# Optimization experiments

Hardware: AMD Instinct MI355X
Metric: run time of the kernel (lower is better)

## Reference

```python
import jax, jax.numpy as jnp
import numpy as np

N_NODES = 50000
HEADS1 = 4
NEG_SLOPE = 0.2
EPS = 1e-16


def gat_conv(x, edge_index, W, att_src, att_dst, bias, heads, out_ch, concat):
    # edge_index: [2, E] with self-loops already appended by caller
    src, dst = edge_index[0], edge_index[1]
    N = x.shape[0]
    h = (x @ W).reshape(N, heads, out_ch)                      # [N, H, C]
    a_src = jnp.sum(h * att_src, axis=-1)                      # [N, H]
    a_dst = jnp.sum(h * att_dst, axis=-1)                      # [N, H]
    e = a_src[src] + a_dst[dst]                                # [E, H]
    e = jnp.where(e > 0, e, NEG_SLOPE * e)                     # leaky_relu
    m = jax.ops.segment_max(e, dst, num_segments=N)            # [N, H]
    alpha = jnp.exp(e - m[dst])                                # [E, H]
    denom = jax.ops.segment_sum(alpha, dst, num_segments=N)    # [N, H]
    alpha = alpha / (denom[dst] + EPS)                         # [E, H]
    msg = alpha[:, :, None] * h[src]                           # [E, H, C]
    out = jax.ops.segment_sum(msg, dst, num_segments=N)        # [N, H, C]
    if concat:
        out = out.reshape(N, heads * out_ch)
    else:
        out = out.mean(axis=1)
    return out + bias, alpha


def setup_inputs() -> dict:
    key = jax.random.key(0)
    ks = jax.random.split(key, 12)
    N, F, H, heads, C, E = N_NODES, 256, 64, HEADS1, 40, 800000
    g = 0.1
    return {
        "x": jax.random.normal(ks[0], (N, F), dtype=jnp.float32),
        "edge_index": jax.random.randint(ks[1], (2, E), 0, N, dtype=jnp.int32),
        "W1": jax.random.normal(ks[2], (F, heads * H), dtype=jnp.float32) * g,
        "att_src1": jax.random.normal(ks[3], (heads, H), dtype=jnp.float32) * g,
        "att_dst1": jax.random.normal(ks[4], (heads, H), dtype=jnp.float32) * g,
        "b1": jnp.zeros((heads * H,), dtype=jnp.float32),
        "W2": jax.random.normal(ks[5], (heads * H, C), dtype=jnp.float32) * g,
        "att_src2": jax.random.normal(ks[6], (1, C), dtype=jnp.float32) * g,
        "att_dst2": jax.random.normal(ks[7], (1, C), dtype=jnp.float32) * g,
        "b2": jnp.zeros((C,), dtype=jnp.float32),
    }


def reference(x, edge_index, W1, att_src1, att_dst1, b1, W2, att_src2, att_dst2, b2):
    N = x.shape[0]
    # add self-loops (PyG GATConv default)
    loops = jnp.arange(N, dtype=edge_index.dtype)
    ei = jnp.concatenate([edge_index, jnp.stack([loops, loops])], axis=1)
    # dropout is identity in eval mode
    h1, alpha = gat_conv(x, ei, W1, att_src1, att_dst1, b1,
                         HEADS1, W1.shape[1] // HEADS1, concat=True)
    h1 = jax.nn.elu(h1)
    h2, _ = gat_conv(h1, ei, W2, att_src2, att_dst2, b2,
                     1, W2.shape[1], concat=False)
    return jax.nn.log_softmax(h2, axis=1), alpha
```

## Files before the change

### kernel.cpp

```cpp
#include <hip/hip_runtime.h>
#include <math.h>

#define N_NODES 50000
#define HC1 256
#define H1 4
#define C2 40
#define C2P 64
#define E0 800000
#define ET 850000
#define NEG_SLOPE 0.2f
#define EPS_A 1e-16f

typedef __bf16 bf16x8 __attribute__((ext_vector_type(8)));
typedef float f32x4 __attribute__((ext_vector_type(4)));
typedef unsigned short u16x8 __attribute__((ext_vector_type(8)));


__device__ inline unsigned short f2bf(float f) {
    unsigned u = __float_as_uint(f);
    return (unsigned short)((u + 0x7FFFu + ((u >> 16) & 1u)) >> 16);
}
__device__ inline float bf_lo(unsigned q) { return __uint_as_float(q << 16); }
__device__ inline float bf_hi(unsigned q) { return __uint_as_float(q & 0xFFFF0000u); }


__global__ void fill_int_kernel(int* __restrict__ p, int n, int v) {
    int i = blockIdx.x * blockDim.x + threadIdx.x;
    if (i < n) p[i] = v;
}

__device__ inline int edge_src(const int* __restrict__ ei, int e) {
    return (e < E0) ? ei[e] : (e - E0);
}
__device__ inline int edge_dst(const int* __restrict__ ei, int e) {
    return (e < E0) ? ei[E0 + e] : (e - E0);
}


#define CV_X 3200000
#define CV_W1 65536
#define CV_W2 16384

__global__ void convert_all_kernel(const float* __restrict__ x,
                                   const float* __restrict__ W1,
                                   const float* __restrict__ W2,
                                   ushort4* __restrict__ xbf,
                                   unsigned short* __restrict__ w1t,
                                   unsigned short* __restrict__ w2t) {
    int tid = blockIdx.x * blockDim.x + threadIdx.x;
    if (tid < CV_X) {
        float4 v = ((const float4*)x)[tid];
        ushort4 w;
        w.x = f2bf(v.x); w.y = f2bf(v.y); w.z = f2bf(v.z); w.w = f2bf(v.w);
        xbf[tid] = w;
    } else if (tid < CV_X + CV_W1) {
        int i = tid - CV_X;
        int n = i >> 8, k = i & 255;
        w1t[i] = f2bf(W1[k * 256 + n]);
    } else if (tid < CV_X + CV_W1 + CV_W2) {
        int i = tid - CV_X - CV_W1;
        int n = i >> 8, k = i & 255;
        w2t[i] = (n < C2) ? f2bf(W2[k * C2 + n]) : (unsigned short)0;
    }
}


__global__ void hist_kernel(const int* __restrict__ ei, int* __restrict__ deg) {
    int e = blockIdx.x * blockDim.x + threadIdx.x;
    if (e >= ET) return;
    atomicAdd(&deg[edge_dst(ei, e)], 1);
}

__global__ __launch_bounds__(256) void scan_block_kernel(const int* __restrict__ deg,
                                                         int* __restrict__ excl,
                                                         int* __restrict__ bsum) {
    __shared__ int tmp[256];
    int t = threadIdx.x;
    int i = blockIdx.x * 256 + t;
    int v = (i < N_NODES) ? deg[i] : 0;
    tmp[t] = v;
    __syncthreads();
#pragma unroll
    for (int o = 1; o < 256; o <<= 1) {
        int x = (t >= o) ? tmp[t - o] : 0;
        __syncthreads();
        tmp[t] += x;
        __syncthreads();
    }
    if (i < N_NODES) excl[i] = tmp[t] - v;
    if (t == 255) bsum[blockIdx.x] = tmp[255];
}

#define NSCAN_B 196

__global__ __launch_bounds__(256) void scan_top_kernel(int* __restrict__ bsum) {
    __shared__ int tmp[256];
    int t = threadIdx.x;
    int v = (t < NSCAN_B) ? bsum[t] : 0;
    tmp[t] = v;
    __syncthreads();
#pragma unroll
    for (int o = 1; o < 256; o <<= 1) {
        int x = (t >= o) ? tmp[t - o] : 0;
        __syncthreads();
        tmp[t] += x;
        __syncthreads();
    }
    if (t < NSCAN_B) bsum[t] = tmp[t] - v;
}

__global__ __launch_bounds__(256) void scan_add_kernel(int* __restrict__ offsets,
                                                       int* __restrict__ cursor,
                                                       const int* __restrict__ bsum) {
    int i = blockIdx.x * 256 + threadIdx.x;
    if (i < N_NODES) {
        int v = offsets[i] + bsum[blockIdx.x];
        offsets[i] = v;
        cursor[i] = v;
    }
    if (i == 0) offsets[N_NODES] = ET;
}

__global__ void scatter_kernel(const int* __restrict__ ei, int* __restrict__ cursor,
                               int2* __restrict__ csr_es) {
    int e = blockIdx.x * blockDim.x + threadIdx.x;
    if (e >= ET) return;
    int d = edge_dst(ei, e);
    int pos = atomicAdd(&cursor[d], 1);
    csr_es[pos] = make_int2(e, edge_src(ei, e));
}


template <int TBM, int TBN, int WROWS, int WCOLS>
__global__ __launch_bounds__(256) void gemm_mfma_kernel(const unsigned short* __restrict__ Abf,
                                                        const unsigned short* __restrict__ Bt,
                                                        unsigned short* __restrict__ Cbf,
                                                        const float* __restrict__ att_s,
                                                        const float* __restrict__ att_d,
                                                        float* __restrict__ a_src_o,
                                                        float* __restrict__ a_dst_o,
                                                        int M, int Nc, int attN, int hstride) {
    static_assert(TBM == WROWS * 64 && TBN == WCOLS * 64, "tile");
    constexpr int LDK = 40;
    __shared__ alignas(16) unsigned short As[TBM * LDK];
    __shared__ alignas(16) unsigned short Bs[TBN * LDK];
    const int t = threadIdx.x;
    const int lane = t & 63;
    const int w = t >> 6;
    const int quad = lane >> 4;
    const int l16 = lane & 15;
    const int wm = (w / WCOLS) * 64;
    const int wn = (w % WCOLS) * 64;
    const int bm = blockIdx.x * TBM;
    const int bn = blockIdx.y * TBN;

    f32x4 acc[4][4] = {};

    for (int k0 = 0; k0 < 256; k0 += 32) {
        __syncthreads();
#pragma unroll
        for (int i = 0; i < TBM / 64; ++i) {
            int idx = t + i * 256;
            int row = idx >> 2, seg = idx & 3;
            u16x8 v = {};
            if (bm + row < M)
                v = *(const u16x8*)(Abf + (size_t)(bm + row) * 256 + k0 + seg * 8);
            *(u16x8*)&As[row * LDK + seg * 8] = v;
        }
#pragma unroll
        for (int i = 0; i < TBN / 64; ++i) {
            int idx = t + i * 256;
            int row = idx >> 2, seg = idx & 3;
            u16x8 v = *(const u16x8*)(Bt + (size_t)(bn + row) * 256 + k0 + seg * 8);
            *(u16x8*)&Bs[row * LDK + seg * 8] = v;
        }
        __syncthreads();

        bf16x8 af[4], bfr[4];
#pragma unroll
        for (int mi = 0; mi < 4; ++mi)
            af[mi] = *(const bf16x8*)&As[(wm + mi * 16 + l16) * LDK + quad * 8];
#pragma unroll
        for (int ni = 0; ni < 4; ++ni)
            bfr[ni] = *(const bf16x8*)&Bs[(wn + ni * 16 + l16) * LDK + quad * 8];
#pragma unroll
        for (int mi = 0; mi < 4; ++mi)
#pragma unroll
            for (int ni = 0; ni < 4; ++ni)
                acc[mi][ni] = __builtin_amdgcn_mfma_f32_16x16x32_bf16(
                    af[mi], bfr[ni], acc[mi][ni], 0, 0, 0);
    }

#pragma unroll
    for (int mi = 0; mi < 4; ++mi)
#pragma unroll
        for (int ni = 0; ni < 4; ++ni)
#pragma unroll
            for (int r = 0; r < 4; ++r) {
                int row = bm + wm + mi * 16 + quad * 4 + r;
                int col = bn + wn + ni * 16 + l16;
                if (row < M)
                    Cbf[(size_t)row * Nc + col] = f2bf(acc[mi][ni][r]);
            }

    float asc[4], adc[4];
#pragma unroll
    for (int ni = 0; ni < 4; ++ni) {
        int col = bn + wn + ni * 16 + l16;
        bool valid = col < attN;
        asc[ni] = valid ? att_s[col] : 0.f;
        adc[ni] = valid ? att_d[col] : 0.f;
    }
    float vs[16], vd[16];
#pragma unroll
    for (int mi = 0; mi < 4; ++mi)
#pragma unroll
        for (int r = 0; r < 4; ++r) {
            float s = 0.f, dd = 0.f;
#pragma unroll
            for (int ni = 0; ni < 4; ++ni) {
                s += acc[mi][ni][r] * asc[ni];
                dd += acc[mi][ni][r] * adc[ni];
            }
            vs[mi * 4 + r] = s;
            vd[mi * 4 + r] = dd;
        }
#pragma unroll
    for (int k = 0; k < 4; ++k) {
        const int o = 1 << k;
        const int b = (l16 >> k) & 1;
#pragma unroll
        for (int j = 0; j < (8 >> k); ++j) {
            float lo = vs[2 * j], hi = vs[2 * j + 1];
            float keep = b ? hi : lo, send = b ? lo : hi;
            vs[j] = keep + __shfl_xor(send, o);
            lo = vd[2 * j]; hi = vd[2 * j + 1];
            keep = b ? hi : lo; send = b ? lo : hi;
            vd[j] = keep + __shfl_xor(send, o);
        }
    }
    {
        int mi = l16 >> 2, r = l16 & 3;
        int row = bm + wm + mi * 16 + quad * 4 + r;
        int head = (bn + wn) >> 6;
        if (row < M) {
            a_src_o[(size_t)row * hstride + head] = vs[0];
            a_dst_o[(size_t)row * hstride + head] = vd[0];
        }
    }
}


__global__ __launch_bounds__(256) void l1_fused_kernel(const int* __restrict__ off,
                                                       const int2* __restrict__ csr_es,
                                                       const float4* __restrict__ a_src4,
                                                       const float4* __restrict__ a_dst4,
                                                       const unsigned* __restrict__ h1bf,
                                                       const float* __restrict__ b1,
                                                       float4* __restrict__ alpha_out4,
                                                       unsigned* __restrict__ out1bf) {
    __shared__ int    s_w[4][64];
    __shared__ float4 a_w[4][64];
    int t = threadIdx.x;
    int w = t >> 6, lane = t & 63;
    int d = blockIdx.x * 4 + w;
    int beg = off[d], end = off[d + 1];
    int deg = end - beg;
    int nch = (deg + 63) >> 6;
    int cnt0 = min(deg, 64);
    bool act0 = lane < cnt0;
    float4 ad4 = a_dst4[d];

    int2  es0 = make_int2(0, 0);
    float4 l0 = make_float4(-INFINITY, -INFINITY, -INFINITY, -INFINITY);
    float4 mx = l0;
    for (int cc = 0; cc < nch; ++cc) {
        int idx = beg + cc * 64 + lane;
        float4 l = make_float4(-INFINITY, -INFINITY, -INFINITY, -INFINITY);
        int2 es = make_int2(0, 0);
        if (idx < end) {
            es = csr_es[idx];
            float4 as4 = a_src4[es.y];
            l.x = as4.x + ad4.x; l.x = l.x > 0.f ? l.x : NEG_SLOPE * l.x;
            l.y = as4.y + ad4.y; l.y = l.y > 0.f ? l.y : NEG_SLOPE * l.y;
            l.z = as4.z + ad4.z; l.z = l.z > 0.f ? l.z : NEG_SLOPE * l.z;
            l.w = as4.w + ad4.w; l.w = l.w > 0.f ? l.w : NEG_SLOPE * l.w;
        }
        if (cc == 0) { es0 = es; l0 = l; }
        mx.x = fmaxf(mx.x, l.x); mx.y = fmaxf(mx.y, l.y);
        mx.z = fmaxf(mx.z, l.z); mx.w = fmaxf(mx.w, l.w);
    }
    int rdeg = cnt0;
    for (int o = 1; o < rdeg; o <<= 1) {
        mx.x = fmaxf(mx.x, __shfl_xor(mx.x, o));
        mx.y = fmaxf(mx.y, __shfl_xor(mx.y, o));
        mx.z = fmaxf(mx.z, __shfl_xor(mx.z, o));
        mx.w = fmaxf(mx.w, __shfl_xor(mx.w, o));
    }
    mx.x = __shfl(mx.x, 0); mx.y = __shfl(mx.y, 0);
    mx.z = __shfl(mx.z, 0); mx.w = __shfl(mx.w, 0);

    float4 p0 = make_float4(0.f, 0.f, 0.f, 0.f);
    if (act0) {
        p0.x = __expf(l0.x - mx.x); p0.y = __expf(l0.y - mx.y);
        p0.z = __expf(l0.z - mx.z); p0.w = __expf(l0.w - mx.w);
    }
    float4 sum = p0;
    for (int cc = 1; cc < nch; ++cc) {
        int idx = beg + cc * 64 + lane;
        if (idx < end) {
            int2 es = csr_es[idx];
            float4 as4 = a_src4[es.y];
            float4 l;
            l.x = as4.x + ad4.x; l.x = l.x > 0.f ? l.x : NEG_SLOPE * l.x;
            l.y = as4.y + ad4.y; l.y = l.y > 0.f ? l.y : NEG_SLOPE * l.y;
            l.z = as4.z + ad4.z; l.z = l.z > 0.f ? l.z : NEG_SLOPE * l.z;
            l.w = as4.w + ad4.w; l.w = l.w > 0.f ? l.w : NEG_SLOPE * l.w;
            sum.x += __expf(l.x - mx.x); sum.y += __expf(l.y - mx.y);
            sum.z += __expf(l.z - mx.z); sum.w += __expf(l.w - mx.w);
        }
    }
    for (int o = 1; o < rdeg; o <<= 1) {
        sum.x += __shfl_xor(sum.x, o);
        sum.y += __shfl_xor(sum.y, o);
        sum.z += __shfl_xor(sum.z, o);
        sum.w += __shfl_xor(sum.w, o);
    }
    sum.x = __shfl(sum.x, 0); sum.y = __shfl(sum.y, 0);
    sum.z = __shfl(sum.z, 0); sum.w = __shfl(sum.w, 0);
    float4 inv;
    inv.x = 1.f / (sum.x + EPS_A); inv.y = 1.f / (sum.y + EPS_A);
    inv.z = 1.f / (sum.z + EPS_A); inv.w = 1.f / (sum.w + EPS_A);

    float4 al0;
    al0.x = p0.x * inv.x; al0.y = p0.y * inv.y;
    al0.z = p0.z * inv.z; al0.w = p0.w * inv.w;
    if (act0) {
        alpha_out4[es0.x] = al0;
        s_w[w][lane] = es0.y;
        a_w[w][lane] = al0;
    }
    __syncthreads();

    int head = lane >> 4;
    int base2 = 2 * lane;
    const float* aw = (const float*)&a_w[w][0];
    float4 acc = make_float4(0.f, 0.f, 0.f, 0.f);
    int j = 0;
    for (; j + 4 <= cnt0; j += 4) {
        int s0 = s_w[w][j], s1 = s_w[w][j + 1], s2 = s_w[w][j + 2], s3 = s_w[w][j + 3];
        float A0 = aw[4 * j + head], A1 = aw[4 * j + 4 + head];
        float A2 = aw[4 * j + 8 + head], A3 = aw[4 * j + 12 + head];
        uint2 q0 = *(const uint2*)&h1bf[(size_t)s0 * 128 + base2];
        uint2 q1 = *(const uint2*)&h1bf[(size_t)s1 * 128 + base2];
        uint2 q2 = *(const uint2*)&h1bf[(size_t)s2 * 128 + base2];
        uint2 q3 = *(const uint2*)&h1bf[(size_t)s3 * 128 + base2];
        acc.x += A0 * bf_lo(q0.x) + A1 * bf_lo(q1.x) + A2 * bf_lo(q2.x) + A3 * bf_lo(q3.x);
        acc.y += A0 * bf_hi(q0.x) + A1 * bf_hi(q1.x) + A2 * bf_hi(q2.x) + A3 * bf_hi(q3.x);
        acc.z += A0 * bf_lo(q0.y) + A1 * bf_lo(q1.y) + A2 * bf_lo(q2.y) + A3 * bf_lo(q3.y);
        acc.w += A0 * bf_hi(q0.y) + A1 * bf_hi(q1.y) + A2 * bf_hi(q2.y) + A3 * bf_hi(q3.y);
    }
    for (; j < cnt0; ++j) {
        int s = s_w[w][j];
        float A = aw[4 * j + head];
        uint2 q = *(const uint2*)&h1bf[(size_t)s * 128 + base2];
        acc.x += A * bf_lo(q.x); acc.y += A * bf_hi(q.x);
        acc.z += A * bf_lo(q.y); acc.w += A * bf_hi(q.y);
    }

    for (int cc = 1; cc < nch; ++cc) {
        int idx = beg + cc * 64 + lane;
        int ms = 0;
        float4 ma = make_float4(0.f, 0.f, 0.f, 0.f);
        if (idx < end) {
            int2 es = csr_es[idx];
            ms = es.y;
            float4 as4 = a_src4[es.y];
            float4 l;
            l.x = as4.x + ad4.x; l.x = l.x > 0.f ? l.x : NEG_SLOPE * l.x;
            l.y = as4.y + ad4.y; l.y = l.y > 0.f ? l.y : NEG_SLOPE * l.y;
            l.z = as4.z + ad4.z; l.z = l.z > 0.f ? l.z : NEG_SLOPE * l.z;
            l.w = as4.w + ad4.w; l.w = l.w > 0.f ? l.w : NEG_SLOPE * l.w;
            ma.x = __expf(l.x - mx.x) * inv.x;
            ma.y = __expf(l.y - mx.y) * inv.y;
            ma.z = __expf(l.z - mx.z) * inv.z;
            ma.w = __expf(l.w - mx.w) * inv.w;
            alpha_out4[es.x] = ma;
        }
        int cnt = min(64, deg - cc * 64);
        for (int jj = 0; jj < cnt; ++jj) {
            int s = __shfl(ms, jj);
            float h0 = __shfl(ma.x, jj), h1 = __shfl(ma.y, jj);
            float h2 = __shfl(ma.z, jj), h3 = __shfl(ma.w, jj);
            float A = (head & 2) ? ((head & 1) ? h3 : h2) : ((head & 1) ? h1 : h0);
            uint2 q = *(const uint2*)&h1bf[(size_t)s * 128 + base2];
            acc.x += A * bf_lo(q.x); acc.y += A * bf_hi(q.x);
            acc.z += A * bf_lo(q.y); acc.w += A * bf_hi(q.y);
        }
    }

    float4 bb = *(const float4*)&b1[4 * lane];
    float v0 = acc.x + bb.x, v1 = acc.y + bb.y, v2 = acc.z + bb.z, v3 = acc.w + bb.w;
    v0 = v0 > 0.f ? v0 : __expf(v0) - 1.f;
    v1 = v1 > 0.f ? v1 : __expf(v1) - 1.f;
    v2 = v2 > 0.f ? v2 : __expf(v2) - 1.f;
    v3 = v3 > 0.f ? v3 : __expf(v3) - 1.f;
    uint2 qo;
    qo.x = ((unsigned)f2bf(v1) << 16) | (unsigned)f2bf(v0);
    qo.y = ((unsigned)f2bf(v3) << 16) | (unsigned)f2bf(v2);
    *(uint2*)&out1bf[(size_t)d * 128 + base2] = qo;
}


__global__ __launch_bounds__(256) void l2_fused_kernel(const int* __restrict__ off,
                                                       const int2* __restrict__ csr_es,
                                                       const float* __restrict__ a_src,
                                                       const float* __restrict__ a_dst,
                                                       const unsigned* __restrict__ h2bf,
                                                       const float* __restrict__ b2,
                                                       float* __restrict__ out) {
    int t = threadIdx.x;
    int lane = t & 63;
    int d = blockIdx.x * 4 + (t >> 6);
    if (d >= N_NODES) return;
    int beg = off[d], end = off[d + 1];
    int deg = end - beg;
    float ad = a_dst[d];
    int nch = (deg + 63) >> 6;

    float elc[4]; int sc[4];
    float mx = -INFINITY;
    for (int cc = 0; cc < nch; ++cc) {
        int idx = beg + cc * 64 + lane;
        float el = -INFINITY; int s = 0;
        if (idx < end) {
            int2 es = csr_es[idx];
            s = es.y;
            el = a_src[s] + ad;
            el = el > 0.f ? el : NEG_SLOPE * el;
        }
        if (cc < 4) { elc[cc] = el; sc[cc] = s; }
        mx = fmaxf(mx, el);
    }
    int rdeg = min(deg, 64);
    for (int o = 1; o < rdeg; o <<= 1) mx = fmaxf(mx, __shfl_xor(mx, o));
    mx = __shfl(mx, 0);

    float sum = 0.f;
    for (int cc = 0; cc < nch; ++cc) {
        int idx = beg + cc * 64 + lane;
        float p = 0.f;
        if (cc < 4) {
            p = (idx < end) ? __expf(elc[cc] - mx) : 0.f;
            elc[cc] = p;
        } else if (idx < end) {
            int2 es = csr_es[idx];
            float el = a_src[es.y] + ad;
            el = el > 0.f ? el : NEG_SLOPE * el;
            p = __expf(el - mx);
        }
        sum += p;
    }
    for (int o = 1; o < rdeg; o <<= 1) sum += __shfl_xor(sum, o);
    sum = __shfl(sum, 0);
    float inv = 1.f / (sum + EPS_A);

    int half = lane >> 5, li = lane & 31;
    float acc0 = 0.f, acc1 = 0.f;
    for (int cc = 0; cc < nch; ++cc) {
        int cnt = min(64, deg - cc * 64);
        int my_s; float my_a;
        if (cc < 4) {
            my_s = sc[cc];
            my_a = elc[cc];
        } else {
            int idx = beg + cc * 64 + lane;
            my_s = 0; my_a = 0.f;
            if (idx < end) {
                int2 es = csr_es[idx];
                my_s = es.y;
                float el = a_src[es.y] + ad;
                el = el > 0.f ? el : NEG_SLOPE * el;
                my_a = __expf(el - mx);
            }
        }
        for (int j = 0; j < cnt; j += 2) {
            int jj = j + half;
            int s = __shfl(my_s, jj);
            float a = __shfl(my_a, jj);
            if (jj < cnt) {
                unsigned q = h2bf[(size_t)s * 32 + li];
                acc0 += a * bf_lo(q);
                acc1 += a * bf_hi(q);
            }
        }
    }
    acc0 += __shfl_xor(acc0, 32);
    acc1 += __shfl_xor(acc1, 32);
    acc0 *= inv;
    acc1 *= inv;
    bool act = li < 20;
    float v0 = act ? acc0 + b2[2 * li]     : -INFINITY;
    float v1 = act ? acc1 + b2[2 * li + 1] : -INFINITY;
    float mmx = fmaxf(v0, v1);
#pragma unroll
    for (int o = 16; o; o >>= 1) mmx = fmaxf(mmx, __shfl_xor(mmx, o));
    float ex = act ? __expf(v0 - mmx) + __expf(v1 - mmx) : 0.f;
#pragma unroll
    for (int o = 16; o; o >>= 1) ex += __shfl_xor(ex, o);
    float ls = __logf(ex);
    if (act && half == 0)
        *(float2*)&out[(size_t)d * C2 + 2 * li] = make_float2(v0 - mmx - ls, v1 - mmx - ls);
}


extern "C" void kernel_launch(void* const* d_in, const int* in_sizes, int n_in,
                              void* d_out, int out_size, void* d_ws, size_t ws_size,
                              hipStream_t stream) {
    const float* x   = (const float*)d_in[0];
    const int*   ei  = (const int*)d_in[1];
    const float* W1  = (const float*)d_in[2];
    const float* as1 = (const float*)d_in[3];
    const float* ad1 = (const float*)d_in[4];
    const float* b1  = (const float*)d_in[5];
    const float* W2  = (const float*)d_in[6];
    const float* as2 = (const float*)d_in[7];
    const float* ad2 = (const float*)d_in[8];
    const float* b2  = (const float*)d_in[9];

    float* out   = (float*)d_out;
    float* alpha = out + (size_t)N_NODES * C2;

    unsigned* u32    = (unsigned*)d_ws;
    unsigned* h1bf   = u32;
    unsigned* xbf    = h1bf + 6400000;
    unsigned* h2bf   = xbf + 6400000;
    unsigned* w1t    = h2bf + 1600000;
    unsigned* w2t    = w1t + 32768;
    float* a_src1    = (float*)(w2t + 8192);
    float* a_dst1    = a_src1 + 200000;
    float* a_src2    = a_dst1 + 200000;
    float* a_dst2    = a_src2 + 50000;
    int*   deg       = (int*)(a_dst2 + 50000);
    int*   offs      = deg + 50000;
    int*   cursor    = offs + 50001;
    int*   bsum      = cursor + 50000;
    int2*  csr_es    = (int2*)(bsum + 257);
    unsigned* out1bf = xbf;

    const int TB = 256;
    const int EB = (ET + TB - 1) / TB;

    fill_int_kernel<<<(N_NODES + TB - 1) / TB, TB, 0, stream>>>(deg, N_NODES, 0);
    hist_kernel<<<EB, TB, 0, stream>>>(ei, deg);
    scan_block_kernel<<<NSCAN_B, TB, 0, stream>>>(deg, offs, bsum);
    scan_top_kernel<<<1, TB, 0, stream>>>(bsum);
    scan_add_kernel<<<NSCAN_B, TB, 0, stream>>>(offs, cursor, bsum);
    scatter_kernel<<<EB, TB, 0, stream>>>(ei, cursor, csr_es);

    convert_all_kernel<<<(CV_X + CV_W1 + CV_W2 + TB - 1) / TB, TB, 0, stream>>>(
        x, W1, W2, (ushort4*)xbf, (unsigned short*)w1t, (unsigned short*)w2t);

    gemm_mfma_kernel<128, 128, 2, 2><<<dim3((N_NODES + 127) / 128, 2), TB, 0, stream>>>(
        (const unsigned short*)xbf, (const unsigned short*)w1t, (unsigned short*)h1bf,
        as1, ad1, a_src1, a_dst1, N_NODES, HC1, 256, H1);
    l1_fused_kernel<<<N_NODES / 4, TB, 0, stream>>>(offs, csr_es,
                                                    (const float4*)a_src1,
                                                    (const float4*)a_dst1,
                                                    h1bf, b1, (float4*)alpha, out1bf);

    gemm_mfma_kernel<256, 64, 4, 1><<<dim3((N_NODES + 255) / 256, 1), TB, 0, stream>>>(
        (const unsigned short*)out1bf, (const unsigned short*)w2t, (unsigned short*)h2bf,
        as2, ad2, a_src2, a_dst2, N_NODES, C2P, C2, 1);
    l2_fused_kernel<<<(N_NODES + 3) / 4, TB, 0, stream>>>(offs, csr_es, a_src2, a_dst2,
                                                          h2bf, b2, out);
}
```

Baseline: 382.0 us.

## Split GAT aggregation across half-waves with wider loads and fuse degree zeroing

In layer-1 aggregation each half-wave now handles alternate edges and loads 16-byte rows (8 bf16 per lane), with a cross-half shuffle reduction at the end. The layer-2 kernel merges the softmax-sum and aggregation passes into one pass, staging (src, p) pairs in LDS so neighbor rows can be fetched two at a time. The degree-zeroing fill kernel is folded into the conversion kernel to remove one launch. These changes aim to raise memory-level parallelism and cut redundant passes over the edges, at the cost of an extra reduction, some LDS traffic, and a layer-2 kernel that no longer guards d >= N_NODES (safe only because N_NODES is divisible by 4).

```diff
diff --git a/kernel.cpp b/kernel.cpp
--- a/kernel.cpp
+++ b/kernel.cpp
@@ -24,11 +24,6 @@
 __device__ inline float bf_hi(unsigned q) { return __uint_as_float(q & 0xFFFF0000u); }
 
 
-__global__ void fill_int_kernel(int* __restrict__ p, int n, int v) {
-    int i = blockIdx.x * blockDim.x + threadIdx.x;
-    if (i < n) p[i] = v;
-}
-
 __device__ inline int edge_src(const int* __restrict__ ei, int e) {
     return (e < E0) ? ei[e] : (e - E0);
 }
@@ -40,13 +35,15 @@
 #define CV_X 3200000
 #define CV_W1 65536
 #define CV_W2 16384
+#define CV_TOT (CV_X + CV_W1 + CV_W2 + N_NODES)
 
 __global__ void convert_all_kernel(const float* __restrict__ x,
                                    const float* __restrict__ W1,
                                    const float* __restrict__ W2,
                                    ushort4* __restrict__ xbf,
                                    unsigned short* __restrict__ w1t,
-                                   unsigned short* __restrict__ w2t) {
+                                   unsigned short* __restrict__ w2t,
+                                   int* __restrict__ deg) {
     int tid = blockIdx.x * blockDim.x + threadIdx.x;
     if (tid < CV_X) {
         float4 v = ((const float4*)x)[tid];
@@ -61,6 +58,8 @@
         int i = tid - CV_X - CV_W1;
         int n = i >> 8, k = i & 255;
         w2t[i] = (n < C2) ? f2bf(W2[k * C2 + n]) : (unsigned short)0;
+    } else if (tid < CV_TOT) {
+        deg[tid - CV_X - CV_W1 - CV_W2] = 0;
     }
 }
 
@@ -342,30 +341,33 @@
     }
     __syncthreads();
 
-    int head = lane >> 4;
-    int base2 = 2 * lane;
+    int hf = lane >> 5, li = lane & 31;
+    int headc = li >> 3;
     const float* aw = (const float*)&a_w[w][0];
-    float4 acc = make_float4(0.f, 0.f, 0.f, 0.f);
-    int j = 0;
-    for (; j + 4 <= cnt0; j += 4) {
-        int s0 = s_w[w][j], s1 = s_w[w][j + 1], s2 = s_w[w][j + 2], s3 = s_w[w][j + 3];
-        float A0 = aw[4 * j + head], A1 = aw[4 * j + 4 + head];
-        float A2 = aw[4 * j + 8 + head], A3 = aw[4 * j + 12 + head];
-        uint2 q0 = *(const uint2*)&h1bf[(size_t)s0 * 128 + base2];
-        uint2 q1 = *(const uint2*)&h1bf[(size_t)s1 * 128 + base2];
-        uint2 q2 = *(const uint2*)&h1bf[(size_t)s2 * 128 + base2];
-        uint2 q3 = *(const uint2*)&h1bf[(size_t)s3 * 128 + base2];
-        acc.x += A0 * bf_lo(q0.x) + A1 * bf_lo(q1.x) + A2 * bf_lo(q2.x) + A3 * bf_lo(q3.x);
-        acc.y += A0 * bf_hi(q0.x) + A1 * bf_hi(q1.x) + A2 * bf_hi(q2.x) + A3 * bf_hi(q3.x);
-        acc.z += A0 * bf_lo(q0.y) + A1 * bf_lo(q1.y) + A2 * bf_lo(q2.y) + A3 * bf_lo(q3.y);
-        acc.w += A0 * bf_hi(q0.y) + A1 * bf_hi(q1.y) + A2 * bf_hi(q2.y) + A3 * bf_hi(q3.y);
-    }
-    for (; j < cnt0; ++j) {
+    float ac[8] = {};
+    int j = hf;
+    for (; j + 2 < cnt0; j += 4) {
+        int s0 = s_w[w][j], s1 = s_w[w][j + 2];
+        float A0 = aw[4 * j + headc], A1 = aw[4 * (j + 2) + headc];
+        uint4 q0 = *(const uint4*)&h1bf[(size_t)s0 * 128 + 4 * li];
+        uint4 q1 = *(const uint4*)&h1bf[(size_t)s1 * 128 + 4 * li];
+        ac[0] += A0 * bf_lo(q0.x) + A1 * bf_lo(q1.x);
+        ac[1] += A0 * bf_hi(q0.x) + A1 * bf_hi(q1.x);
+        ac[2] += A0 * bf_lo(q0.y) + A1 * bf_lo(q1.y);
+        ac[3] += A0 * bf_hi(q0.y) + A1 * bf_hi(q1.y);
+        ac[4] += A0 * bf_lo(q0.z) + A1 * bf_lo(q1.z);
+        ac[5] += A0 * bf_hi(q0.z) + A1 * bf_hi(q1.z);
+        ac[6] += A0 * bf_lo(q0.w) + A1 * bf_lo(q1.w);
+        ac[7] += A0 * bf_hi(q0.w) + A1 * bf_hi(q1.w);
+    }
+    for (; j < cnt0; j += 2) {
         int s = s_w[w][j];
-        float A = aw[4 * j + head];
-        uint2 q = *(const uint2*)&h1bf[(size_t)s * 128 + base2];
-        acc.x += A * bf_lo(q.x); acc.y += A * bf_hi(q.x);
-        acc.z += A * bf_lo(q.y); acc.w += A * bf_hi(q.y);
+        float A = aw[4 * j + headc];
+        uint4 q = *(const uint4*)&h1bf[(size_t)s * 128 + 4 * li];
+        ac[0] += A * bf_lo(q.x); ac[1] += A * bf_hi(q.x);
+        ac[2] += A * bf_lo(q.y); ac[3] += A * bf_hi(q.y);
+        ac[4] += A * bf_lo(q.z); ac[5] += A * bf_hi(q.z);
+        ac[6] += A * bf_lo(q.w); ac[7] += A * bf_hi(q.w);
     }
 
     for (int cc = 1; cc < nch; ++cc) {
@@ -388,27 +390,43 @@
             alpha_out4[es.x] = ma;
         }
         int cnt = min(64, deg - cc * 64);
-        for (int jj = 0; jj < cnt; ++jj) {
+        for (int jj = hf; jj < cnt; jj += 2) {
             int s = __shfl(ms, jj);
-            float h0 = __shfl(ma.x, jj), h1 = __shfl(ma.y, jj);
-            float h2 = __shfl(ma.z, jj), h3 = __shfl(ma.w, jj);
-            float A = (head & 2) ? ((head & 1) ? h3 : h2) : ((head & 1) ? h1 : h0);
-            uint2 q = *(const uint2*)&h1bf[(size_t)s * 128 + base2];
-            acc.x += A * bf_lo(q.x); acc.y += A * bf_hi(q.x);
-            acc.z += A * bf_lo(q.y); acc.w += A * bf_hi(q.y);
-        }
-    }
-
-    float4 bb = *(const float4*)&b1[4 * lane];
-    float v0 = acc.x + bb.x, v1 = acc.y + bb.y, v2 = acc.z + bb.z, v3 = acc.w + bb.w;
-    v0 = v0 > 0.f ? v0 : __expf(v0) - 1.f;
-    v1 = v1 > 0.f ? v1 : __expf(v1) - 1.f;
-    v2 = v2 > 0.f ? v2 : __expf(v2) - 1.f;
-    v3 = v3 > 0.f ? v3 : __expf(v3) - 1.f;
-    uint2 qo;
-    qo.x = ((unsigned)f2bf(v1) << 16) | (unsigned)f2bf(v0);
-    qo.y = ((unsigned)f2bf(v3) << 16) | (unsigned)f2bf(v2);
-    *(uint2*)&out1bf[(size_t)d * 128 + base2] = qo;
+            float h0 = __shfl(ma.x, jj), h1v = __shfl(ma.y, jj);
+            float h2v = __shfl(ma.z, jj), h3 = __shfl(ma.w, jj);
+            float A = (headc & 2) ? ((headc & 1) ? h3 : h2v) : ((headc & 1) ? h1v : h0);
+            uint4 q = *(const uint4*)&h1bf[(size_t)s * 128 + 4 * li];
+            ac[0] += A * bf_lo(q.x); ac[1] += A * bf_hi(q.x);
+            ac[2] += A * bf_lo(q.y); ac[3] += A * bf_hi(q.y);
+            ac[4] += A * bf_lo(q.z); ac[5] += A * bf_hi(q.z);
+            ac[6] += A * bf_lo(q.w); ac[7] += A * bf_hi(q.w);
+        }
+    }
+
+#pragma unroll
+    for (int c = 0; c < 8; ++c) ac[c] += __shfl_xor(ac[c], 32);
+    if (hf == 0) {
+        float4 bb0 = *(const float4*)&b1[8 * li];
+        float4 bb1 = *(const float4*)&b1[8 * li + 4];
+        float v0 = ac[0] + bb0.x, v1 = ac[1] + bb0.y;
+        float v2 = ac[2] + bb0.z, v3 = ac[3] + bb0.w;
+        float v4 = ac[4] + bb1.x, v5 = ac[5] + bb1.y;
+        float v6 = ac[6] + bb1.z, v7 = ac[7] + bb1.w;
+        v0 = v0 > 0.f ? v0 : __expf(v0) - 1.f;
+        v1 = v1 > 0.f ? v1 : __expf(v1) - 1.f;
+        v2 = v2 > 0.f ? v2 : __expf(v2) - 1.f;
+        v3 = v3 > 0.f ? v3 : __expf(v3) - 1.f;
+        v4 = v4 > 0.f ? v4 : __expf(v4) - 1.f;
+        v5 = v5 > 0.f ? v5 : __expf(v5) - 1.f;
+        v6 = v6 > 0.f ? v6 : __expf(v6) - 1.f;
+        v7 = v7 > 0.f ? v7 : __expf(v7) - 1.f;
+        uint4 qo;
+        qo.x = ((unsigned)f2bf(v1) << 16) | (unsigned)f2bf(v0);
+        qo.y = ((unsigned)f2bf(v3) << 16) | (unsigned)f2bf(v2);
+        qo.z = ((unsigned)f2bf(v5) << 16) | (unsigned)f2bf(v4);
+        qo.w = ((unsigned)f2bf(v7) << 16) | (unsigned)f2bf(v6);
+        *(uint4*)&out1bf[(size_t)d * 128 + 4 * li] = qo;
+    }
 }
 
 
@@ -419,16 +437,17 @@
                                                        const unsigned* __restrict__ h2bf,
                                                        const float* __restrict__ b2,
                                                        float* __restrict__ out) {
+    __shared__ uint2 sp_w[4][64];
     int t = threadIdx.x;
-    int lane = t & 63;
-    int d = blockIdx.x * 4 + (t >> 6);
-    if (d >= N_NODES) return;
+    int w = t >> 6, lane = t & 63;
+    int d = blockIdx.x * 4 + w;
     int beg = off[d], end = off[d + 1];
     int deg = end - beg;
     float ad = a_dst[d];
     int nch = (deg + 63) >> 6;
-
-    float elc[4]; int sc[4];
+    int rdeg = min(deg, 64);
+
+    int s0r = 0; float el0 = -INFINITY;
     float mx = -INFINITY;
     for (int cc = 0; cc < nch; ++cc) {
         int idx = beg + cc * 64 + lane;
@@ -439,62 +458,53 @@
             el = a_src[s] + ad;
             el = el > 0.f ? el : NEG_SLOPE * el;
         }
-        if (cc < 4) { elc[cc] = el; sc[cc] = s; }
+        if (cc == 0) { el0 = el; s0r = s; }
         mx = fmaxf(mx, el);
     }
-    int rdeg = min(deg, 64);
     for (int o = 1; o < rdeg; o <<= 1) mx = fmaxf(mx, __shfl_xor(mx, o));
     mx = __shfl(mx, 0);
 
-    float sum = 0.f;
+    int hf = lane >> 5, li = lane & 31;
+    float sum = 0.f, acc0 = 0.f, acc1 = 0.f;
     for (int cc = 0; cc < nch; ++cc) {
-        int idx = beg + cc * 64 + lane;
-        float p = 0.f;
-        if (cc < 4) {
-            p = (idx < end) ? __expf(elc[cc] - mx) : 0.f;
-            elc[cc] = p;
-        } else if (idx < end) {
-            int2 es = csr_es[idx];
-            float el = a_src[es.y] + ad;
-            el = el > 0.f ? el : NEG_SLOPE * el;
-            p = __expf(el - mx);
+        int cnt = min(64, deg - cc * 64);
+        float p = 0.f; int s = 0;
+        if (cc == 0) {
+            s = s0r;
+            p = (lane < cnt) ? __expf(el0 - mx) : 0.f;
+        } else {
+            int idx = beg + cc * 64 + lane;
+            if (idx < end) {
+                int2 es = csr_es[idx];
+                s = es.y;
+                float el = a_src[s] + ad;
+                el = el > 0.f ? el : NEG_SLOPE * el;
+                p = __expf(el - mx);
+            }
         }
         sum += p;
+        if (lane < cnt) sp_w[w][lane] = make_uint2((unsigned)s, __float_as_uint(p));
+        int j = hf;
+        for (; j + 2 < cnt; j += 4) {
+            uint2 e0 = sp_w[w][j], e1 = sp_w[w][j + 2];
+            float A0 = __uint_as_float(e0.y), A1 = __uint_as_float(e1.y);
+            unsigned q0 = h2bf[(size_t)e0.x * 32 + li];
+            unsigned q1 = h2bf[(size_t)e1.x * 32 + li];
+            acc0 += A0 * bf_lo(q0) + A1 * bf_lo(q1);
+            acc1 += A0 * bf_hi(q0) + A1 * bf_hi(q1);
+        }
+        for (; j < cnt; j += 2) {
+            uint2 e0 = sp_w[w][j];
+            float A0 = __uint_as_float(e0.y);
+            unsigned q = h2bf[(size_t)e0.x * 32 + li];
+            acc0 += A0 * bf_lo(q);
+            acc1 += A0 * bf_hi(q);
+        }
     }
     for (int o = 1; o < rdeg; o <<= 1) sum += __shfl_xor(sum, o);
     sum = __shfl(sum, 0);
     float inv = 1.f / (sum + EPS_A);
 
-    int half = lane >> 5, li = lane & 31;
-    float acc0 = 0.f, acc1 = 0.f;
-    for (int cc = 0; cc < nch; ++cc) {
-        int cnt = min(64, deg - cc * 64);
-        int my_s; float my_a;
-        if (cc < 4) {
-            my_s = sc[cc];
-            my_a = elc[cc];
-        } else {
-            int idx = beg + cc * 64 + lane;
-            my_s = 0; my_a = 0.f;
-            if (idx < end) {
-                int2 es = csr_es[idx];
-                my_s = es.y;
-                float el = a_src[es.y] + ad;
-                el = el > 0.f ? el : NEG_SLOPE * el;
-                my_a = __expf(el - mx);
-            }
-        }
-        for (int j = 0; j < cnt; j += 2) {
-            int jj = j + half;
-            int s = __shfl(my_s, jj);
-            float a = __shfl(my_a, jj);
-            if (jj < cnt) {
-                unsigned q = h2bf[(size_t)s * 32 + li];
-                acc0 += a * bf_lo(q);
-                acc1 += a * bf_hi(q);
-            }
-        }
-    }
     acc0 += __shfl_xor(acc0, 32);
     acc1 += __shfl_xor(acc1, 32);
     acc0 *= inv;
@@ -509,7 +519,7 @@
 #pragma unroll
     for (int o = 16; o; o >>= 1) ex += __shfl_xor(ex, o);
     float ls = __logf(ex);
-    if (act && half == 0)
+    if (act && hf == 0)
         *(float2*)&out[(size_t)d * C2 + 2 * li] = make_float2(v0 - mmx - ls, v1 - mmx - ls);
 }
 
@@ -551,15 +561,14 @@
     const int TB = 256;
     const int EB = (ET + TB - 1) / TB;
 
-    fill_int_kernel<<<(N_NODES + TB - 1) / TB, TB, 0, stream>>>(deg, N_NODES, 0);
+    convert_all_kernel<<<(CV_TOT + TB - 1) / TB, TB, 0, stream>>>(
+        x, W1, W2, (ushort4*)xbf, (unsigned short*)w1t, (unsigned short*)w2t, deg);
+
     hist_kernel<<<EB, TB, 0, stream>>>(ei, deg);
     scan_block_kernel<<<NSCAN_B, TB, 0, stream>>>(deg, offs, bsum);
     scan_top_kernel<<<1, TB, 0, stream>>>(bsum);
     scan_add_kernel<<<NSCAN_B, TB, 0, stream>>>(offs, cursor, bsum);
     scatter_kernel<<<EB, TB, 0, stream>>>(ei, cursor, csr_es);
-
-    convert_all_kernel<<<(CV_X + CV_W1 + CV_W2 + TB - 1) / TB, TB, 0, stream>>>(
-        x, W1, W2, (ushort4*)xbf, (unsigned short*)w1t, (unsigned short*)w2t);
 
     gemm_mfma_kernel<128, 128, 2, 2><<<dim3((N_NODES + 127) / 128, 2), TB, 0, stream>>>(
         (const unsigned short*)xbf, (const unsigned short*)w1t, (unsigned short*)h1bf,
```

After: 365.9 us. -4.2%, faster.
